# Performance work log

Measured on AMD Instinct MI355X. Metric: run time of the kernel, lower is better.

The kernel has to match this reference:

```python
import jax, jax.numpy as jnp
import numpy as np

B, S, D, H = 2, 2048, 1024, 16
HD = D // H  # 64


def setup_inputs() -> dict:
    key = jax.random.key(0)
    ks = jax.random.split(key, 10)
    sc = 1.0 / np.sqrt(D)
    return {
        "decoder_hs": jax.random.normal(ks[0], (B, S, D), jnp.float32),
        "encoder_hs": jax.random.normal(ks[1], (B, S, D), jnp.float32),
        "Wq": jax.random.normal(ks[2], (D, D), jnp.float32) * sc,
        "bq": jax.random.normal(ks[3], (D,), jnp.float32) * 0.02,
        "Wk": jax.random.normal(ks[4], (D, D), jnp.float32) * sc,
        "bk": jax.random.normal(ks[5], (D,), jnp.float32) * 0.02,
        "Wv": jax.random.normal(ks[6], (D, D), jnp.float32) * sc,
        "bv": jax.random.normal(ks[7], (D,), jnp.float32) * 0.02,
        "Wp": jax.random.normal(ks[8], (D, D), jnp.float32) * sc,
        "bp": jax.random.normal(ks[9], (D,), jnp.float32) * 0.02,
    }


def reference(decoder_hs, encoder_hs, Wq, bq, Wk, bk, Wv, bv, Wp, bp):
    b, s, d = decoder_hs.shape
    # torch nn.Linear: y = x @ W.T + b, W is [out, in]
    q = decoder_hs @ Wq.T + bq
    k = encoder_hs @ Wk.T + bk
    v = encoder_hs @ Wv.T + bv
    # head split: [b, s, d] -> [b, h, s, hd]
    q = q.reshape(b, s, H, HD).transpose(0, 2, 1, 3)
    k = k.reshape(b, s, H, HD).transpose(0, 2, 1, 3)
    v = v.reshape(b, s, H, HD).transpose(0, 2, 1, 3)
    scale = 1.0 / np.sqrt(HD).astype(np.float32)
    att = jnp.einsum('bhqd,bhkd->bhqk', q, k) * scale
    att = jax.nn.softmax(att, axis=-1)
    y = jnp.einsum('bhqk,bhkd->bhqd', att, v)
    y = y.transpose(0, 2, 1, 3).reshape(b, s, d)
    return y @ Wp.T + bp
```

## Files before the change

### kernel.cpp

```cpp
#include <hip/hip_runtime.h>
#include <hip/hip_bf16.h>
#include <cstdint>
#include <cstddef>

#define BB 2
#define SS 2048
#define DD 1024
#define HH 16
#define HD 64

typedef __attribute__((ext_vector_type(8))) short bf16x8;
typedef __attribute__((ext_vector_type(4))) float f32x4;
typedef __attribute__((ext_vector_type(16))) float f32x16;

#define GLL(g, l) __builtin_amdgcn_global_load_lds( \
    (const __attribute__((address_space(1))) void*)(g), \
    (__attribute__((address_space(3))) void*)(l), 16, 0, 0)

__device__ __forceinline__ short f2bf_fast(float f) {
    uint32_t u = __float_as_uint(f);
    u += 0x7FFF + ((u >> 16) & 1);
    return (short)(u >> 16);
}
__device__ __forceinline__ uint32_t pack_bf2(float a, float b) {
    uint32_t ua = __float_as_uint(a), ub = __float_as_uint(b);
    ua += 0x7FFF + ((ua >> 16) & 1);
    ub += 0x7FFF + ((ub >> 16) & 1);
    return (ua >> 16) | (ub & 0xFFFF0000u);
}
__device__ __forceinline__ uint32_t cvtpk_bf2(float a, float b) {
    uint32_t r;
    asm("v_cvt_pk_bf16_f32 %0, %1, %2" : "=v"(r) : "v"(a), "v"(b));
    return r;
}
__device__ __forceinline__ void pl32swap(uint32_t& a, uint32_t& b) {
    asm("v_permlane32_swap_b32 %0, %1" : "+v"(a), "+v"(b));
}
__device__ __forceinline__ bf16x8 cvt8(const float* __restrict__ p) {
    float4 a = *(const float4*)p;
    float4 b = *(const float4*)(p + 4);
    union { uint32_t d[4]; bf16x8 v; } r;
    r.d[0] = pack_bf2(a.x, a.y);
    r.d[1] = pack_bf2(a.z, a.w);
    r.d[2] = pack_bf2(b.x, b.y);
    r.d[3] = pack_bf2(b.z, b.w);
    return r.v;
}

__global__ __launch_bounds__(256) void cvt6_kernel(
    const float* __restrict__ s0, const float* __restrict__ s1,
    const float* __restrict__ s2, const float* __restrict__ s3,
    const float* __restrict__ s4, const float* __restrict__ s5,
    short* __restrict__ d0, short* __restrict__ d1, short* __restrict__ d2,
    short* __restrict__ d3, short* __restrict__ d4, short* __restrict__ d5)
{
    const int id = blockIdx.x * 256 + threadIdx.x;
    const float* s; short* d; size_t off;
    if (id < 1048576) {
        int e = id >> 19;
        off = (size_t)(id & 524287) * 8;
        s = e ? s1 : s0;  d = e ? d1 : d0;
    } else {
        int j = id - 1048576;
        int w = j >> 17;
        off = (size_t)(j & 131071) * 8;
        s = (w == 0) ? s2 : (w == 1) ? s3 : (w == 2) ? s4 : s5;
        d = (w == 0) ? d2 : (w == 1) ? d3 : (w == 2) ? d4 : d5;
    }
    bf16x8 r = cvt8(s + off);
    *(uint4*)(d + off) = *(uint4*)&r;
}

template<int BF>
__global__ __launch_bounds__(256, 3) void qkv_gemm_kernel(
    const void* __restrict__ dec, const void* __restrict__ enc,
    const void* __restrict__ Wq, const void* __restrict__ Wk,
    const void* __restrict__ Wv,
    const float* __restrict__ bq, const float* __restrict__ bk,
    const float* __restrict__ bv,
    short* __restrict__ Qo, short* __restrict__ Ko, short* __restrict__ Vo)
{
    __shared__ short As[128 * 32];
    __shared__ short Bs[128 * 32];

    const int z = blockIdx.z;
    const void* Xv = (z == 0) ? dec : enc;
    const void* Wp_ = (z == 0) ? Wq : (z == 1) ? Wk : Wv;
    const float* bias = (z == 0) ? bq : (z == 1) ? bk : bv;
    short* Yo = (z == 0) ? Qo : (z == 1) ? Ko : Vo;
    const float qs = (z == 0) ? (0.125f * 1.44269504088896f) : 1.0f;

    const int t = threadIdx.x;
    const int lane = t & 63, wv = t >> 6;
    const int lr = lane & 15, quad = lane >> 4;
    const int wm = wv >> 1, wn = wv & 1;
    const int m0 = blockIdx.y * 128;
    const int n0 = blockIdx.x * 128;
    const int K = DD;

    f32x4 acc[4][4];
    #pragma unroll
    for (int i = 0; i < 4; i++)
        #pragma unroll
        for (int j = 0; j < 4; j++) acc[i][j] = (f32x4){0.f, 0.f, 0.f, 0.f};

    for (int kb = 0; kb < K; kb += 32) {
        __syncthreads();
        if (BF) {
            const short* Xb = (const short*)Xv;
            const short* Wb = (const short*)Wp_;
            #pragma unroll
            for (int c = 0; c < 2; c++) {
                int r0 = wv * 32 + c * 16;
                int r = r0 + (lane >> 2), ch = (lane & 3) * 8;
                GLL(Xb + (size_t)(m0 + r) * K + kb + ch, &As[r0 * 32]);
                GLL(Wb + (size_t)(n0 + r) * K + kb + ch, &Bs[r0 * 32]);
            }
        } else {
            const float* Xf = (const float*)Xv;
            const float* Wf = (const float*)Wp_;
            #pragma unroll
            for (int c = 0; c < 2; c++) {
                int id = t + c * 256;
                int r = id >> 2, c8 = (id & 3) * 8;
                *(bf16x8*)&As[r * 32 + c8] = cvt8(Xf + (size_t)(m0 + r) * K + kb + c8);
                *(bf16x8*)&Bs[r * 32 + c8] = cvt8(Wf + (size_t)(n0 + r) * K + kb + c8);
            }
        }
        __syncthreads();

        bf16x8 af[4], bfr[4];
        #pragma unroll
        for (int mi = 0; mi < 4; mi++)
            af[mi] = *(const bf16x8*)&As[(wm * 64 + mi * 16 + lr) * 32 + quad * 8];
        #pragma unroll
        for (int ni = 0; ni < 4; ni++)
            bfr[ni] = *(const bf16x8*)&Bs[(wn * 64 + ni * 16 + lr) * 32 + quad * 8];
        #pragma unroll
        for (int mi = 0; mi < 4; mi++)
            #pragma unroll
            for (int ni = 0; ni < 4; ni++)
                acc[mi][ni] = __builtin_amdgcn_mfma_f32_16x16x32_bf16(
                    af[mi], bfr[ni], acc[mi][ni], 0, 0, 0);
    }

    if (z < 2) {
        #pragma unroll
        for (int ni = 0; ni < 4; ni++) {
            int col = n0 + wn * 64 + ni * 16 + lr;
            int h = col >> 6, hd = col & 63;
            float bvv = bias[col];
            #pragma unroll
            for (int mi = 0; mi < 4; mi++) {
                #pragma unroll
                for (int r2 = 0; r2 < 4; r2++) {
                    int row = m0 + wm * 64 + mi * 16 + quad * 4 + r2;
                    int b = row >> 11, s = row & 2047;
                    float v = (acc[mi][ni][r2] + bvv) * qs;
                    size_t off = ((size_t)(b * HH + h) * SS + s) * HD + hd;
                    Yo[off] = f2bf_fast(v);
                }
            }
        }
    } else {
        #pragma unroll
        for (int ni = 0; ni < 4; ni++) {
            int col = n0 + wn * 64 + ni * 16 + lr;
            int h = col >> 6, hd = col & 63;
            float bvv = bias[col];
            #pragma unroll
            for (int mi = 0; mi < 4; mi++) {
                int s0 = m0 + wm * 64 + mi * 16 + quad * 4;
                int b = s0 >> 11, s = s0 & 2047;
                union { uint32_t d[2]; } u;
                u.d[0] = pack_bf2(acc[mi][ni][0] + bvv, acc[mi][ni][1] + bvv);
                u.d[1] = pack_bf2(acc[mi][ni][2] + bvv, acc[mi][ni][3] + bvv);
                size_t off = ((size_t)(b * HH + h) * HD + hd) * SS + s;
                *(uint2*)(Yo + off) = *(uint2*)&u;
            }
        }
    }
}

template<int WBF>
__global__ __launch_bounds__(256, 2) void proj_gemm_kernel(
    const short* __restrict__ X,
    const void* __restrict__ W, const float* __restrict__ bias,
    float* __restrict__ Y)
{
    __shared__ short As[64 * 32];
    __shared__ short Bs[128 * 32];

    const int t = threadIdx.x;
    const int lane = t & 63, wv = t >> 6;
    const int lr = lane & 15, quad = lane >> 4;
    const int wm = wv >> 1, wn = wv & 1;
    const int m0 = blockIdx.y * 64;
    const int n0 = blockIdx.x * 128;
    const int K = DD, N = DD;

    f32x4 acc[2][4];
    #pragma unroll
    for (int i = 0; i < 2; i++)
        #pragma unroll
        for (int j = 0; j < 4; j++) acc[i][j] = (f32x4){0.f, 0.f, 0.f, 0.f};

    for (int kb = 0; kb < K; kb += 32) {
        __syncthreads();
        {
            int r0 = wv * 16;
            int r = r0 + (lane >> 2), ch = (lane & 3) * 8;
            GLL(X + (size_t)(m0 + r) * K + kb + ch, &As[r0 * 32]);
        }
        if (WBF) {
            const short* Wb = (const short*)W;
            #pragma unroll
            for (int c = 0; c < 2; c++) {
                int r0 = wv * 32 + c * 16;
                int r = r0 + (lane >> 2), ch = (lane & 3) * 8;
                GLL(Wb + (size_t)(n0 + r) * K + kb + ch, &Bs[r0 * 32]);
            }
        } else {
            const float* Wf = (const float*)W;
            #pragma unroll
            for (int c = 0; c < 2; c++) {
                int id = t + c * 256;
                int r = id >> 2, c8 = (id & 3) * 8;
                *(bf16x8*)&Bs[r * 32 + c8] = cvt8(Wf + (size_t)(n0 + r) * K + kb + c8);
            }
        }
        __syncthreads();

        bf16x8 af[2], bfr[4];
        #pragma unroll
        for (int mi = 0; mi < 2; mi++)
            af[mi] = *(const bf16x8*)&As[(wm * 32 + mi * 16 + lr) * 32 + quad * 8];
        #pragma unroll
        for (int ni = 0; ni < 4; ni++)
            bfr[ni] = *(const bf16x8*)&Bs[(wn * 64 + ni * 16 + lr) * 32 + quad * 8];
        #pragma unroll
        for (int mi = 0; mi < 2; mi++)
            #pragma unroll
            for (int ni = 0; ni < 4; ni++)
                acc[mi][ni] = __builtin_amdgcn_mfma_f32_16x16x32_bf16(
                    af[mi], bfr[ni], acc[mi][ni], 0, 0, 0);
    }

    #pragma unroll
    for (int ni = 0; ni < 4; ni++) {
        int col = n0 + wn * 64 + ni * 16 + lr;
        float bvv = bias[col];
        #pragma unroll
        for (int mi = 0; mi < 2; mi++) {
            #pragma unroll
            for (int r2 = 0; r2 < 4; r2++) {
                int row = m0 + wm * 32 + mi * 16 + quad * 4 + r2;
                Y[(size_t)row * N + col] = acc[mi][ni][r2] + bvv;
            }
        }
    }
}

__global__ __launch_bounds__(256, 2) void attn_kernel(
    const short* __restrict__ Q,
    const short* __restrict__ Kgl,
    const short* __restrict__ Vt_g,
    short* __restrict__ Y)
{
    __shared__ short Ks[2][128][64];
    __shared__ short Vt[2][64][128];

    const int t = threadIdx.x;
    const int lane = t & 63, w = t >> 6;
    const int lq = lane & 31, hf = lane >> 5;
    const int e = lq & 7;

    const int bid = blockIdx.x;
    const int slot = bid >> 3;
    const int bh = ((slot >> 4) << 3) + (bid & 7);
    const int qt = slot & 15;
    const int b = bh >> 4, h = bh & 15;

    const int q = qt * 128 + w * 32 + lq;
    const short* Qp = Q + ((size_t)bh * SS + q) * HD;
    bf16x8 qf[4];
    #pragma unroll
    for (int j = 0; j < 4; j++)
        qf[j] = *(const bf16x8*)(Qp + j * 16 + hf * 8);

    f32x16 o[2];
    #pragma unroll
    for (int i = 0; i < 16; i++) { o[0][i] = 0.f; o[1][i] = 0.f; }
    f32x4 vsum = (f32x4){0.f, 0.f, 0.f, 0.f};

    const short* Kb = Kgl + (size_t)bh * SS * HD;
    const short* Vb = Vt_g + (size_t)bh * HD * SS;

    auto stage = [&](int kt1, int nb) {
        #pragma unroll
        for (int c = 0; c < 4; c++) {
            int r0 = w * 32 + c * 8;
            int r  = r0 + (lane >> 3);
            int sc = ((lane & 7) ^ (r & 7)) * 8;
            GLL(Kb + (size_t)(kt1 * 128 + r) * 64 + sc, &Ks[nb][r0][0]);
        }
        #pragma unroll
        for (int c = 0; c < 4; c++) {
            int h0 = w * 16 + c * 4;
            int hd = h0 + (lane >> 4);
            int s16 = (lane & 15) ^ (hd & 7);
            GLL(Vb + (size_t)hd * SS + kt1 * 128 + s16 * 8, &Vt[nb][h0][0]);
        }
    };

    stage(0, 0);
    __syncthreads();

    int cur = 0;
    for (int kt = 0; kt < SS / 128; kt++) {
        if (kt + 1 < SS / 128) stage(kt + 1, cur ^ 1);

        bf16x8 pb[4][2];
        #pragma unroll
        for (int s = 0; s < 4; s++) {
            const short* krow = &Ks[cur][s * 32 + lq][0];
            f32x16 sc = (f32x16){0.f,0.f,0.f,0.f,0.f,0.f,0.f,0.f,
                                 0.f,0.f,0.f,0.f,0.f,0.f,0.f,0.f};
            __builtin_amdgcn_s_setprio(1);
            #pragma unroll
            for (int j = 0; j < 4; j++) {
                bf16x8 kf = *(const bf16x8*)&krow[((j * 2 + hf) ^ e) * 8];
                sc = __builtin_amdgcn_mfma_f32_32x32x16_bf16(kf, qf[j], sc, 0, 0, 0);
            }
            __builtin_amdgcn_s_setprio(0);

            float ev[16];
            #pragma unroll
            for (int i = 0; i < 16; i++) ev[i] = __builtin_amdgcn_exp2f(sc[i]);
            #pragma unroll
            for (int r = 0; r < 4; r++)
                vsum += (f32x4){ev[4*r], ev[4*r+1], ev[4*r+2], ev[4*r+3]};
            uint32_t dw[8];
            #pragma unroll
            for (int i = 0; i < 8; i++) dw[i] = cvtpk_bf2(ev[2*i], ev[2*i+1]);
            pl32swap(dw[0], dw[2]); pl32swap(dw[1], dw[3]);
            pl32swap(dw[4], dw[6]); pl32swap(dw[5], dw[7]);
            union { uint32_t u[4]; bf16x8 v; } f0, f1;
            f0.u[0] = dw[0]; f0.u[1] = dw[1]; f0.u[2] = dw[2]; f0.u[3] = dw[3];
            f1.u[0] = dw[4]; f1.u[1] = dw[5]; f1.u[2] = dw[6]; f1.u[3] = dw[7];
            pb[s][0] = f0.v; pb[s][1] = f1.v;
        }

        __builtin_amdgcn_s_setprio(1);
        #pragma unroll
        for (int ds = 0; ds < 2; ds++) {
            const short* vrow = &Vt[cur][ds * 32 + lq][0];
            #pragma unroll
            for (int s = 0; s < 4; s++)
                #pragma unroll
                for (int c = 0; c < 2; c++) {
                    bf16x8 va = *(const bf16x8*)&vrow[((s * 4 + c * 2 + hf) ^ e) * 8];
                    o[ds] = __builtin_amdgcn_mfma_f32_32x32x16_bf16(
                        va, pb[s][c], o[ds], 0, 0, 0);
                }
        }
        __builtin_amdgcn_s_setprio(0);

        __syncthreads();
        cur ^= 1;
    }

    float lsum = (vsum[0] + vsum[1]) + (vsum[2] + vsum[3]);
    lsum += __shfl_xor(lsum, 32, 64);
    float inv = 1.0f / lsum;

    short* Yp = Y + ((size_t)b * SS + q) * DD + h * 64 + hf * 4;
    #pragma unroll
    for (int ds = 0; ds < 2; ds++)
        #pragma unroll
        for (int rr = 0; rr < 4; rr++) {
            union { uint32_t d[2]; } u;
            u.d[0] = pack_bf2(o[ds][rr*4+0] * inv, o[ds][rr*4+1] * inv);
            u.d[1] = pack_bf2(o[ds][rr*4+2] * inv, o[ds][rr*4+3] * inv);
            *(uint2*)(Yp + ds * 32 + rr * 8) = *(uint2*)&u;
        }
}

extern "C" void kernel_launch(void* const* d_in, const int* in_sizes, int n_in,
                              void* d_out, int out_size, void* d_ws, size_t ws_size,
                              hipStream_t stream) {
    const float* dec = (const float*)d_in[0];
    const float* enc = (const float*)d_in[1];
    const float* Wq  = (const float*)d_in[2];
    const float* bq  = (const float*)d_in[3];
    const float* Wk  = (const float*)d_in[4];
    const float* bk  = (const float*)d_in[5];
    const float* Wv  = (const float*)d_in[6];
    const float* bv  = (const float*)d_in[7];
    const float* Wp  = (const float*)d_in[8];
    const float* bp  = (const float*)d_in[9];

    const size_t per = (size_t)BB * HH * SS * HD;
    const size_t wsz = (size_t)DD * DD;
    short* ws = (short*)d_ws;
    short* Qb  = ws;
    short* Kb  = ws + per;
    short* Vtb = ws + 2 * per;
    short* Yb  = ws + 3 * per;

    dim3 qkv_grid(DD / 128, (BB * SS) / 128, 3);
    dim3 proj_grid(DD / 128, (BB * SS) / 64);
    const int attn_blocks = BB * HH * (SS / 128);
    const int cvt_blocks = (2 * 524288 + 4 * 131072) / 256;

    const size_t need = (6 * per + 4 * wsz) * sizeof(short);
    if (ws_size >= need) {
        short* decb = ws + 4 * per;
        short* encb = ws + 5 * per;
        short* Wqb  = ws + 6 * per;
        short* Wkb  = Wqb + wsz;
        short* Wvb  = Wqb + 2 * wsz;
        short* Wpb  = Wqb + 3 * wsz;
        cvt6_kernel<<<cvt_blocks, 256, 0, stream>>>(
            dec, enc, Wq, Wk, Wv, Wp, decb, encb, Wqb, Wkb, Wvb, Wpb);
        qkv_gemm_kernel<1><<<qkv_grid, 256, 0, stream>>>(
            decb, encb, Wqb, Wkb, Wvb, bq, bk, bv, Qb, Kb, Vtb);
        attn_kernel<<<attn_blocks, 256, 0, stream>>>(Qb, Kb, Vtb, Yb);
        proj_gemm_kernel<1><<<proj_grid, 256, 0, stream>>>(Yb, Wpb, bp, (float*)d_out);
    } else {
        qkv_gemm_kernel<0><<<qkv_grid, 256, 0, stream>>>(
            dec, enc, Wq, Wk, Wv, bq, bk, bv, Qb, Kb, Vtb);
        attn_kernel<<<attn_blocks, 256, 0, stream>>>(Qb, Kb, Vtb, Yb);
        proj_gemm_kernel<0><<<proj_grid, 256, 0, stream>>>(Yb, Wp, bp, (float*)d_out);
    }
}
```

Measured before the change: 203.4 us.

## Add 256x128-tile QKV GEMM with triple-buffered async LDS pipeline

Replaces the bf16 QKV projection GEMM with a new kernel that uses 256x128 output tiles, so each block covers more work and reuses the weight tile across twice the rows. K-slices are prefetched two steps ahead into triple-buffered LDS via global_load_lds, with vmcnt waits and a single barrier per step, which removes the load/compute serialization of the old kernel. MFMA sections are wrapped in s_setprio. The larger tiles raise register and LDS use (occupancy bound of 2), and the grid becomes half as many blocks (384), which may underfill the CUs. The fp32 fallback path is split out as its own kernel without functional change.

```diff
diff --git a/kernel.cpp b/kernel.cpp
--- a/kernel.cpp
+++ b/kernel.cpp
@@ -71,11 +71,137 @@
     *(uint4*)(d + off) = *(uint4*)&r;
 }
 
-template<int BF>
-__global__ __launch_bounds__(256, 3) void qkv_gemm_kernel(
-    const void* __restrict__ dec, const void* __restrict__ enc,
-    const void* __restrict__ Wq, const void* __restrict__ Wk,
-    const void* __restrict__ Wv,
+__global__ __launch_bounds__(256, 2) void qkv_gemm256_kernel(
+    const short* __restrict__ dec, const short* __restrict__ enc,
+    const short* __restrict__ Wq, const short* __restrict__ Wk,
+    const short* __restrict__ Wv,
+    const float* __restrict__ bq, const float* __restrict__ bk,
+    const float* __restrict__ bv,
+    short* __restrict__ Qo, short* __restrict__ Ko, short* __restrict__ Vo)
+{
+    __shared__ short As3[3][256 * 32];
+    __shared__ short Bs3[3][128 * 32];
+
+    const int z = blockIdx.z;
+    const short* Xb = (z == 0) ? dec : enc;
+    const short* Wb = (z == 0) ? Wq : (z == 1) ? Wk : Wv;
+    const float* bias = (z == 0) ? bq : (z == 1) ? bk : bv;
+    short* Yo = (z == 0) ? Qo : (z == 1) ? Ko : Vo;
+    const float qs = (z == 0) ? (0.125f * 1.44269504088896f) : 1.0f;
+
+    const int t = threadIdx.x;
+    const int lane = t & 63, wv = t >> 6;
+    const int lr = lane & 15, quad = lane >> 4;
+    const int wm = wv >> 1, wn = wv & 1;
+    const int m0 = blockIdx.y * 256;
+    const int n0 = blockIdx.x * 128;
+    const int K = DD;
+
+    f32x4 acc[8][4];
+    #pragma unroll
+    for (int i = 0; i < 8; i++)
+        #pragma unroll
+        for (int j = 0; j < 4; j++) acc[i][j] = (f32x4){0.f, 0.f, 0.f, 0.f};
+
+    auto stage = [&](int kb, short* Ab, short* Bb) {
+        #pragma unroll
+        for (int r = 0; r < 4; r++) {
+            int r0 = wv * 16 + r * 64;
+            int row = r0 + (lane >> 2), ch = (lane & 3) * 8;
+            GLL(Xb + (size_t)(m0 + row) * K + kb + ch, Ab + r0 * 32);
+        }
+        #pragma unroll
+        for (int r = 0; r < 2; r++) {
+            int r0 = wv * 16 + r * 64;
+            int row = r0 + (lane >> 2), ch = (lane & 3) * 8;
+            GLL(Wb + (size_t)(n0 + row) * K + kb + ch, Bb + r0 * 32);
+        }
+    };
+
+    short *pa = &As3[0][0], *p1 = &As3[1][0], *p2 = &As3[2][0];
+    short *qb = &Bs3[0][0], *q1 = &Bs3[1][0], *q2 = &Bs3[2][0];
+
+    stage(0, pa, qb);
+    stage(32, p1, q1);
+    asm volatile("s_waitcnt vmcnt(6)" ::: "memory");
+    __builtin_amdgcn_s_barrier();
+    asm volatile("" ::: "memory");
+
+    for (int kt = 0; kt < 32; kt++) {
+        if (kt < 30) stage((kt + 2) * 32, p2, q2);
+
+        bf16x8 af[8], bfv[4];
+        #pragma unroll
+        for (int mi = 0; mi < 8; mi++)
+            af[mi] = *(const bf16x8*)&pa[(wm * 128 + mi * 16 + lr) * 32 + quad * 8];
+        #pragma unroll
+        for (int ni = 0; ni < 4; ni++)
+            bfv[ni] = *(const bf16x8*)&qb[(wn * 64 + ni * 16 + lr) * 32 + quad * 8];
+
+        __builtin_amdgcn_s_setprio(1);
+        #pragma unroll
+        for (int mi = 0; mi < 8; mi++)
+            #pragma unroll
+            for (int ni = 0; ni < 4; ni++)
+                acc[mi][ni] = __builtin_amdgcn_mfma_f32_16x16x32_bf16(
+                    af[mi], bfv[ni], acc[mi][ni], 0, 0, 0);
+        __builtin_amdgcn_s_setprio(0);
+
+        if (kt < 30) {
+            asm volatile("s_waitcnt vmcnt(6)" ::: "memory");
+            __builtin_amdgcn_s_barrier();
+            asm volatile("" ::: "memory");
+        } else if (kt == 30) {
+            asm volatile("s_waitcnt vmcnt(0)" ::: "memory");
+            __builtin_amdgcn_s_barrier();
+            asm volatile("" ::: "memory");
+        }
+        short* tp = pa; pa = p1; p1 = p2; p2 = tp;
+        tp = qb; qb = q1; q1 = q2; q2 = tp;
+    }
+
+    if (z < 2) {
+        #pragma unroll
+        for (int ni = 0; ni < 4; ni++) {
+            int col = n0 + wn * 64 + ni * 16 + lr;
+            int h = col >> 6, hd = col & 63;
+            float bvv = bias[col];
+            #pragma unroll
+            for (int mi = 0; mi < 8; mi++) {
+                #pragma unroll
+                for (int r2 = 0; r2 < 4; r2++) {
+                    int row = m0 + wm * 128 + mi * 16 + quad * 4 + r2;
+                    int b = row >> 11, s = row & 2047;
+                    float v = (acc[mi][ni][r2] + bvv) * qs;
+                    size_t off = ((size_t)(b * HH + h) * SS + s) * HD + hd;
+                    Yo[off] = f2bf_fast(v);
+                }
+            }
+        }
+    } else {
+        #pragma unroll
+        for (int ni = 0; ni < 4; ni++) {
+            int col = n0 + wn * 64 + ni * 16 + lr;
+            int h = col >> 6, hd = col & 63;
+            float bvv = bias[col];
+            #pragma unroll
+            for (int mi = 0; mi < 8; mi++) {
+                int s0 = m0 + wm * 128 + mi * 16 + quad * 4;
+                int b = s0 >> 11, s = s0 & 2047;
+                union { uint32_t d[2]; } u;
+                u.d[0] = pack_bf2(acc[mi][ni][0] + bvv, acc[mi][ni][1] + bvv);
+                u.d[1] = pack_bf2(acc[mi][ni][2] + bvv, acc[mi][ni][3] + bvv);
+                size_t off = ((size_t)(b * HH + h) * HD + hd) * SS + s;
+                *(uint2*)(Yo + off) = *(uint2*)&u;
+            }
+        }
+    }
+}
+
+__global__ __launch_bounds__(256, 3) void qkv_gemm_f32_kernel(
+    const float* __restrict__ dec, const float* __restrict__ enc,
+    const float* __restrict__ Wq, const float* __restrict__ Wk,
+    const float* __restrict__ Wv,
     const float* __restrict__ bq, const float* __restrict__ bk,
     const float* __restrict__ bv,
     short* __restrict__ Qo, short* __restrict__ Ko, short* __restrict__ Vo)
@@ -84,8 +210,8 @@
     __shared__ short Bs[128 * 32];
 
     const int z = blockIdx.z;
-    const void* Xv = (z == 0) ? dec : enc;
-    const void* Wp_ = (z == 0) ? Wq : (z == 1) ? Wk : Wv;
+    const float* Xf = (z == 0) ? dec : enc;
+    const float* Wf = (z == 0) ? Wq : (z == 1) ? Wk : Wv;
     const float* bias = (z == 0) ? bq : (z == 1) ? bk : bv;
     short* Yo = (z == 0) ? Qo : (z == 1) ? Ko : Vo;
     const float qs = (z == 0) ? (0.125f * 1.44269504088896f) : 1.0f;
@@ -106,26 +232,12 @@
 
     for (int kb = 0; kb < K; kb += 32) {
         __syncthreads();
-        if (BF) {
-            const short* Xb = (const short*)Xv;
-            const short* Wb = (const short*)Wp_;
-            #pragma unroll
-            for (int c = 0; c < 2; c++) {
-                int r0 = wv * 32 + c * 16;
-                int r = r0 + (lane >> 2), ch = (lane & 3) * 8;
-                GLL(Xb + (size_t)(m0 + r) * K + kb + ch, &As[r0 * 32]);
-                GLL(Wb + (size_t)(n0 + r) * K + kb + ch, &Bs[r0 * 32]);
-            }
-        } else {
-            const float* Xf = (const float*)Xv;
-            const float* Wf = (const float*)Wp_;
-            #pragma unroll
-            for (int c = 0; c < 2; c++) {
-                int id = t + c * 256;
-                int r = id >> 2, c8 = (id & 3) * 8;
-                *(bf16x8*)&As[r * 32 + c8] = cvt8(Xf + (size_t)(m0 + r) * K + kb + c8);
-                *(bf16x8*)&Bs[r * 32 + c8] = cvt8(Wf + (size_t)(n0 + r) * K + kb + c8);
-            }
+        #pragma unroll
+        for (int c = 0; c < 2; c++) {
+            int id = t + c * 256;
+            int r = id >> 2, c8 = (id & 3) * 8;
+            *(bf16x8*)&As[r * 32 + c8] = cvt8(Xf + (size_t)(m0 + r) * K + kb + c8);
+            *(bf16x8*)&Bs[r * 32 + c8] = cvt8(Wf + (size_t)(n0 + r) * K + kb + c8);
         }
         __syncthreads();
 
@@ -408,6 +520,7 @@
     short* Vtb = ws + 2 * per;
     short* Yb  = ws + 3 * per;
 
+    dim3 qkv256_grid(DD / 128, (BB * SS) / 256, 3);
     dim3 qkv_grid(DD / 128, (BB * SS) / 128, 3);
     dim3 proj_grid(DD / 128, (BB * SS) / 64);
     const int attn_blocks = BB * HH * (SS / 128);
@@ -423,12 +536,12 @@
         short* Wpb  = Wqb + 3 * wsz;
         cvt6_kernel<<<cvt_blocks, 256, 0, stream>>>(
             dec, enc, Wq, Wk, Wv, Wp, decb, encb, Wqb, Wkb, Wvb, Wpb);
-        qkv_gemm_kernel<1><<<qkv_grid, 256, 0, stream>>>(
+        qkv_gemm256_kernel<<<qkv256_grid, 256, 0, stream>>>(
             decb, encb, Wqb, Wkb, Wvb, bq, bk, bv, Qb, Kb, Vtb);
         attn_kernel<<<attn_blocks, 256, 0, stream>>>(Qb, Kb, Vtb, Yb);
         proj_gemm_kernel<1><<<proj_grid, 256, 0, stream>>>(Yb, Wpb, bp, (float*)d_out);
     } else {
-        qkv_gemm_kernel<0><<<qkv_grid, 256, 0, stream>>>(
+        qkv_gemm_f32_kernel<<<qkv_grid, 256, 0, stream>>>(
             dec, enc, Wq, Wk, Wv, bq, bk, bv, Qb, Kb, Vtb);
         attn_kernel<<<attn_blocks, 256, 0, stream>>>(Qb, Kb, Vtb, Yb);
         proj_gemm_kernel<0><<<proj_grid, 256, 0, stream>>>(Yb, Wp, bp, (float*)d_out);
```

Result: slower. 208.2 us (+2.4%).
